# Kernel tuning notes

Measured on AMD Instinct MI355X. Metric: run time of the kernel, lower is better.

Reference implementation:

```python
import jax, jax.numpy as jnp
import numpy as np

DIM = 512
HEADS = 16
HD = DIM // HEADS            # head_dim = 32
WH, WW = 8, 8                # window_size
D0, D1 = 2, 2                # dilated_size
TWH, TWW = WH * D0, WW * D1  # total_window_size = 16,16
SCALE = HD ** -0.5


def _wpart(x, wh, ww):
    # (B,H,W,C) -> (B * H/wh * W/ww, wh, ww, C)
    B, H, W, C = x.shape
    x = x.reshape(B, H // wh, wh, W // ww, ww, C)
    return x.transpose(0, 1, 3, 2, 4, 5).reshape(-1, wh, ww, C)


def _wrev(win, wh, ww, H, W):
    # (nW*B, wh, ww, C) -> (B, H, W, C)
    C = win.shape[-1]
    B = win.shape[0] // ((H // wh) * (W // ww))
    x = win.reshape(B, H // wh, W // ww, wh, ww, C).transpose(0, 1, 3, 2, 4, 5)
    return x.reshape(B, H, W, C)


def _rope2(x):
    # 2D RoPE over a (B, WH, WW, HD) window: first half of HD rotated by row
    # position, second half by column position (axial rotary embedding).
    d = HD // 2
    inv = 1.0 / (10000.0 ** (jnp.arange(0, d, 2, dtype=jnp.float32) / d))  # (d/2,)

    def rot(xp, ang):
        x1, x2 = xp[..., 0::2], xp[..., 1::2]
        c, s = jnp.cos(ang), jnp.sin(ang)
        return jnp.stack([x1 * c - x2 * s, x1 * s + x2 * c], axis=-1).reshape(xp.shape)

    ah = (jnp.arange(WH, dtype=jnp.float32)[:, None] * inv)[:, None, :]  # (WH,1,d/2)
    aw = (jnp.arange(WW, dtype=jnp.float32)[:, None] * inv)[None, :, :]  # (1,WW,d/2)
    return jnp.concatenate([rot(x[..., :d], ah), rot(x[..., d:], aw)], axis=-1)


def _forward(x, qkv_w, qkv_b, proj_w, proj_b):
    B, H, W, C = x.shape
    # partition into total windows, then dilated regrouping
    xw = _wpart(x, TWH, TWW)                                   # (B_, 16, 16, C)
    B_ = xw.shape[0]
    xw = _wpart(xw, D0, D1)                                    # (B_*64, 2, 2, C)
    xw = xw.reshape(B_, WH * WW, D0 * D1, C)
    xw = xw.transpose(0, 2, 1, 3).reshape(B_ * D0 * D1, WH * WW, C)  # (B__, N, C)
    B__, N = xw.shape[0], xw.shape[1]

    qkv = (xw @ qkv_w.T + qkv_b).reshape(B__, N, 3, HEADS, HD).transpose(2, 0, 3, 1, 4)
    q, k, v = qkv[0], qkv[1], qkv[2]                           # (B__, HEADS, N, HD)

    q = _rope2(q.reshape(-1, WH, WW, HD)).reshape(B__, HEADS, N, HD) * SCALE
    k = _rope2(k.reshape(-1, WH, WW, HD)).reshape(B__, HEADS, N, HD)

    attn = jax.nn.softmax(jnp.einsum('bhnd,bhmd->bhnm', q, k), axis=-1)
    out = jnp.einsum('bhnm,bhmd->bhnd', attn, v)               # (B__, HEADS, N, HD)
    out = out.transpose(0, 2, 1, 3).reshape(B__, N, C)

    # undo dilated regrouping, then undo total-window partition
    out = out.reshape(B_, D0 * D1, N, C).transpose(0, 2, 1, 3).reshape(-1, D0, D1, C)
    out = _wrev(out, D0, D1, TWH, TWW)                         # (B_, 16, 16, C)
    out = _wrev(out, TWH, TWW, H, W)                           # (B, H, W, C)
    return out @ proj_w.T + proj_b


def setup_inputs() -> dict:
    key = jax.random.key(0)
    k0, k1, k2 = jax.random.split(key, 3)
    x = jax.random.normal(k0, (4, 128, 128, DIM), dtype=jnp.float32)
    qkv_w = jax.random.normal(k1, (3 * DIM, DIM), dtype=jnp.float32) * (DIM ** -0.5)
    qkv_b = jnp.zeros((3 * DIM,), dtype=jnp.float32)
    proj_w = jax.random.normal(k2, (DIM, DIM), dtype=jnp.float32) * (DIM ** -0.5)
    proj_b = jnp.zeros((DIM,), dtype=jnp.float32)
    return {"x": x, "qkv_w": qkv_w, "qkv_b": qkv_b, "proj_w": proj_w, "proj_b": proj_b}


def reference(x, qkv_w, qkv_b, proj_w, proj_b):
    return _forward(x, qkv_w, qkv_b, proj_w, proj_b)
```

## Files before the change

### kernel.cpp

```cpp
#include <hip/hip_runtime.h>
#include <hip/hip_bf16.h>
#include <stdint.h>

#define DIMC  512
#define NHEAD 16
#define HDIM  32
#define NTOK  65536
#define QKVN  1536
static constexpr float SCALE_F = 0.17677669529663687f;

typedef __attribute__((ext_vector_type(4))) float  f32x4;
typedef __attribute__((ext_vector_type(8))) __bf16 bf16x8;

__device__ __forceinline__ uint16_t f2bf(float f) {
  union { float f; uint32_t u; } v; v.f = f;
  return (uint16_t)((v.u + 0x7FFFu + ((v.u >> 16) & 1u)) >> 16);
}

__device__ __forceinline__ void gload_lds16(const void* g, void* l) {
  __builtin_amdgcn_global_load_lds((const __attribute__((address_space(1))) void*)g,
                                   (__attribute__((address_space(3))) void*)l,
                                   16, 0, 0);
}

__global__ void cvt_f32_bf16(const float* __restrict__ src,
                             uint16_t* __restrict__ dst, int n4)
{
  int i = blockIdx.x * blockDim.x + threadIdx.x;
  const int stride = gridDim.x * blockDim.x;
  for (; i < n4; i += stride) {
    const float4 v = ((const float4*)src)[i];
    ushort4 o;
    o.x = f2bf(v.x); o.y = f2bf(v.y); o.z = f2bf(v.z); o.w = f2bf(v.w);
    ((ushort4*)dst)[i] = o;
  }
}

template <bool OUT_F32>
__global__ __launch_bounds__(512, 2)
void gemm256_8ph(const uint16_t* __restrict__ A,
                 const uint16_t* __restrict__ B,
                 const float* __restrict__ bias,
                 void* __restrict__ Cv,
                 int M, int N, int K, int gx)
{
  __shared__ __align__(16) char lds[131072];

  const int tid = threadIdx.x;
  const int l  = tid & 63, w = tid >> 6;
  const int wm = w >> 2,  wn = w & 3;
  const int lm = l & 15,  lq = l >> 4;

  const int nwg = gridDim.x;
  const int qq = nwg >> 3, rr = nwg & 7;
  const int xcd = blockIdx.x & 7, loc = blockIdx.x >> 3;
  const int sw = (xcd < rr ? xcd * (qq + 1) : rr * (qq + 1) + (xcd - rr) * qq) + loc;
  const long m0 = (long)(sw / gx) * 256;
  const long n0 = (long)(sw % gx) * 256;

  const int srow  = tid >> 3;
  const int scolb = (((tid & 7) ^ (srow & 7)) << 4);
  const uint16_t* Ags = A + (m0 + srow) * (long)K + (scolb >> 1);
  const uint16_t* Bgs = B + (n0 + srow) * (long)K + (scolb >> 1);
  char* ldsW = lds + (w << 10);

  auto STAGE = [&](const uint16_t* Gs, int regionOff, int half, int kt) {
    const uint16_t* s0 = Gs + (size_t)(half * 128) * K + kt;
    gload_lds16(s0,                 ldsW + regionOff);
    gload_lds16(s0 + (size_t)64 * K, ldsW + regionOff + 8192);
  };

  const int colx0 = ((lq ^ (lm & 7)) << 4);
  const int aoff0 = (wm * 64 + lm) * 128 + colx0;
  const int aoff1 = (wm * 64 + lm) * 128 + (colx0 ^ 64);
  const int boff0 = (wn * 32 + lm) * 128 + colx0;
  const int boff1 = (wn * 32 + lm) * 128 + (colx0 ^ 64);

  f32x4 acc[2][2][4][2] = {};

#define PHASE(SLOT, QM, QN, STG, VM)                                          \
  {                                                                           \
    const char* Ab = lds + (SLOT) * 65536 + (QM) * 16384;                     \
    const char* Bb = lds + (SLOT) * 65536 + 32768 + (QN) * 16384;             \
    bf16x8 af0[4], af1[4], bq0[2], bq1[2];                                    \
    _Pragma("unroll") for (int i = 0; i < 4; ++i) {                           \
      af0[i] = *(const bf16x8*)(Ab + aoff0 + i * 2048);                       \
      af1[i] = *(const bf16x8*)(Ab + aoff1 + i * 2048);                       \
    }                                                                         \
    _Pragma("unroll") for (int j = 0; j < 2; ++j) {                           \
      bq0[j] = *(const bf16x8*)(Bb + boff0 + j * 2048);                       \
      bq1[j] = *(const bf16x8*)(Bb + boff1 + j * 2048);                       \
    }                                                                         \
    STG;                                                                      \
    __builtin_amdgcn_s_barrier();                                             \
    __builtin_amdgcn_s_setprio(1);                                            \
    _Pragma("unroll") for (int i = 0; i < 4; ++i)                             \
      _Pragma("unroll") for (int j = 0; j < 2; ++j) {                         \
        acc[QM][QN][i][j] = __builtin_amdgcn_mfma_f32_16x16x32_bf16(          \
            af0[i], bq0[j], acc[QM][QN][i][j], 0, 0, 0);                      \
        acc[QM][QN][i][j] = __builtin_amdgcn_mfma_f32_16x16x32_bf16(          \
            af1[i], bq1[j], acc[QM][QN][i][j], 0, 0, 0);                      \
      }                                                                       \
    __builtin_amdgcn_s_setprio(0);                                            \
    if (VM) { asm volatile("s_waitcnt vmcnt(4)" ::: "memory"); }              \
    __builtin_amdgcn_s_barrier();                                             \
  }

  STAGE(Ags, 0,             0, 0);
  STAGE(Bgs, 32768,         0, 0);
  STAGE(Ags, 16384,         1, 0);
  STAGE(Bgs, 49152,         1, 0);
  STAGE(Ags, 65536,         0, 64);
  STAGE(Bgs, 65536 + 32768, 0, 64);
  asm volatile("s_waitcnt vmcnt(4)" ::: "memory");
  __builtin_amdgcn_s_barrier();

  for (int t2 = 0; t2 < K / 64; t2 += 2) {
    const int k1 = (t2 + 1) * 64;
    int k2 = (t2 + 2) * 64; if (k2 >= K) k2 = 0;
    int k3 = (t2 + 3) * 64; if (k3 >= K) k3 = 0;
    PHASE(0, 0, 0, STAGE(Ags, 65536 + 16384, 1, k1), 0)
    PHASE(0, 0, 1, STAGE(Bgs, 65536 + 49152, 1, k1), 0)
    PHASE(0, 1, 0, STAGE(Ags, 0,             0, k2), 0)
    PHASE(0, 1, 1, STAGE(Bgs, 32768,         0, k2), 1)
    PHASE(1, 0, 0, STAGE(Ags, 16384,         1, k2), 0)
    PHASE(1, 0, 1, STAGE(Bgs, 49152,         1, k2), 0)
    PHASE(1, 1, 0, STAGE(Ags, 65536,         0, k3), 0)
    PHASE(1, 1, 1, STAGE(Bgs, 65536 + 32768, 0, k3), 1)
  }
#undef PHASE

#pragma unroll
  for (int qm = 0; qm < 2; ++qm)
#pragma unroll
  for (int qn = 0; qn < 2; ++qn)
#pragma unroll
  for (int i = 0; i < 4; ++i)
#pragma unroll
  for (int j = 0; j < 2; ++j) {
    const long m = m0 + qm * 128 + wm * 64 + i * 16 + lq * 4;
    const long n = n0 + qn * 128 + wn * 32 + j * 16 + lm;
    const float bv = bias[n];
#pragma unroll
    for (int r = 0; r < 4; ++r) {
      const float val = acc[qm][qn][i][j][r] + bv;
      if (OUT_F32) ((float*)Cv)[(m + r) * (long)N + n] = val;
      else         ((uint16_t*)Cv)[(m + r) * (long)N + n] = f2bf(val);
    }
  }
}

__global__ void attn_win(const uint16_t* __restrict__ QKV,
                         uint16_t* __restrict__ O)
{
  __shared__ __align__(16) __bf16 Pl[4][64][72];

  const int tid = threadIdx.x;
  const int l  = tid & 63, w = tid >> 6;
  const int lm = l & 15,  lq = l >> 4;
  const int bid = blockIdx.x;
  const int g = bid >> 2;
  const int h = (bid & 3) * 4 + w;

  const int d1 = g & 1, d0 = (g >> 1) & 1;
  const int wx = (g >> 2) & 7, wy = (g >> 5) & 7, bb = g >> 8;
  const long tbase = ((long)(bb * 128 + wy * 16 + d0) * 128) + wx * 16 + d1;

  f32x4 invs;
#pragma unroll
  for (int i = 0; i < 4; ++i)
    invs[i] = exp2f(-1.6609640474436813f * (float)((lq & 1) * 4 + i));

  const int co_q = h * HDIM;
  const int co_k = DIMC + h * HDIM;
  const int co_v = 2 * DIMC + h * HDIM;

  bf16x8 qf[4], kf[4];
#pragma unroll
  for (int f = 0; f < 4; ++f) {
    const int n  = f * 16 + lm;
    const int iy = n >> 3, ix = n & 7;
    const float pos = (lq < 2) ? (float)iy : (float)ix;
    const long t = tbase + iy * 256 + ix * 2;
    const uint16_t* qp = QKV + t * QKVN + co_q + lq * 8;
    const uint16_t* kp = QKV + t * QKVN + co_k + lq * 8;
    {
      bf16x8 raw = *(const bf16x8*)qp, o;
#pragma unroll
      for (int i = 0; i < 4; ++i) {
        float x1 = (float)raw[2 * i], x2 = (float)raw[2 * i + 1];
        float s, c; __sincosf(pos * invs[i], &s, &c);
        o[2 * i]     = (__bf16)((x1 * c - x2 * s) * SCALE_F);
        o[2 * i + 1] = (__bf16)((x1 * s + x2 * c) * SCALE_F);
      }
      qf[f] = o;
    }
    {
      bf16x8 raw = *(const bf16x8*)kp, o;
#pragma unroll
      for (int i = 0; i < 4; ++i) {
        float x1 = (float)raw[2 * i], x2 = (float)raw[2 * i + 1];
        float s, c; __sincosf(pos * invs[i], &s, &c);
        o[2 * i]     = (__bf16)(x1 * c - x2 * s);
        o[2 * i + 1] = (__bf16)(x1 * s + x2 * c);
      }
      kf[f] = o;
    }
  }

  const f32x4 fzero = {0.f, 0.f, 0.f, 0.f};
  f32x4 s[4][4];
#pragma unroll
  for (int mi = 0; mi < 4; ++mi)
#pragma unroll
    for (int ni = 0; ni < 4; ++ni)
      s[mi][ni] = __builtin_amdgcn_mfma_f32_16x16x32_bf16(qf[mi], kf[ni], fzero, 0, 0, 0);

  float rsum[4][4];
#pragma unroll
  for (int mi = 0; mi < 4; ++mi)
#pragma unroll
    for (int r = 0; r < 4; ++r) {
      float m = s[mi][0][r];
#pragma unroll
      for (int ni = 1; ni < 4; ++ni) m = fmaxf(m, s[mi][ni][r]);
      m = fmaxf(m, __shfl_xor(m, 1));
      m = fmaxf(m, __shfl_xor(m, 2));
      m = fmaxf(m, __shfl_xor(m, 4));
      m = fmaxf(m, __shfl_xor(m, 8));
      float sum = 0.f;
#pragma unroll
      for (int ni = 0; ni < 4; ++ni) {
        float p = expf(s[mi][ni][r] - m);
        s[mi][ni][r] = p;
        sum += p;
      }
      sum += __shfl_xor(sum, 1);
      sum += __shfl_xor(sum, 2);
      sum += __shfl_xor(sum, 4);
      sum += __shfl_xor(sum, 8);
      rsum[mi][r] = sum;
    }

#pragma unroll
  for (int mi = 0; mi < 4; ++mi)
#pragma unroll
    for (int ni = 0; ni < 4; ++ni)
#pragma unroll
      for (int r = 0; r < 4; ++r)
        Pl[w][mi * 16 + lq * 4 + r][ni * 16 + lm] = (__bf16)s[mi][ni][r];

  bf16x8 pa[4][2];
#pragma unroll
  for (int mi = 0; mi < 4; ++mi)
#pragma unroll
    for (int kk = 0; kk < 2; ++kk)
      pa[mi][kk] = *(const bf16x8*)(&Pl[w][mi * 16 + lm][kk * 32 + lq * 8]);

  bf16x8 vf[2][2];
#pragma unroll
  for (int kk = 0; kk < 2; ++kk)
#pragma unroll
    for (int n2 = 0; n2 < 2; ++n2) {
      const int nb = kk * 32 + lq * 8;
      const long tb2 = tbase + (long)(nb >> 3) * 256;
      const uint16_t* vp = QKV + co_v + n2 * 16 + lm;
      bf16x8 o;
#pragma unroll
      for (int i = 0; i < 8; ++i)
        o[i] = *(const __bf16*)(vp + (tb2 + 2 * i) * QKVN);
      vf[kk][n2] = o;
    }

  f32x4 oacc[4][2] = {};
#pragma unroll
  for (int kk = 0; kk < 2; ++kk)
#pragma unroll
    for (int mi = 0; mi < 4; ++mi)
#pragma unroll
      for (int n2 = 0; n2 < 2; ++n2)
        oacc[mi][n2] = __builtin_amdgcn_mfma_f32_16x16x32_bf16(
            pa[mi][kk], vf[kk][n2], oacc[mi][n2], 0, 0, 0);

#pragma unroll
  for (int mi = 0; mi < 4; ++mi)
#pragma unroll
    for (int r = 0; r < 4; ++r) {
      const int n = mi * 16 + lq * 4 + r;
      const long t = tbase + (n >> 3) * 256 + (n & 7) * 2;
      const float rinv = 1.0f / rsum[mi][r];
#pragma unroll
      for (int n2 = 0; n2 < 2; ++n2)
        O[t * DIMC + h * HDIM + n2 * 16 + lm] = f2bf(oacc[mi][n2][r] * rinv);
    }
}

extern "C" void kernel_launch(void* const* d_in, const int* in_sizes, int n_in,
                              void* d_out, int out_size, void* d_ws, size_t ws_size,
                              hipStream_t stream)
{
  const float* x      = (const float*)d_in[0];
  const float* qkv_w  = (const float*)d_in[1];
  const float* qkv_b  = (const float*)d_in[2];
  const float* proj_w = (const float*)d_in[3];
  const float* proj_b = (const float*)d_in[4];
  float* out = (float*)d_out;

  uint16_t* xb    = (uint16_t*)d_ws;
  uint16_t* qwb   = xb    + (size_t)NTOK * DIMC;
  uint16_t* pwb   = qwb   + (size_t)QKVN * DIMC;
  uint16_t* qkv   = pwb   + (size_t)DIMC * DIMC;
  uint16_t* attn  = qkv   + (size_t)NTOK * QKVN;

  cvt_f32_bf16<<<2048, 256, 0, stream>>>(x,      xb,  NTOK * DIMC / 4);
  cvt_f32_bf16<<<512,  256, 0, stream>>>(qkv_w,  qwb, QKVN * DIMC / 4);
  cvt_f32_bf16<<<256,  256, 0, stream>>>(proj_w, pwb, DIMC * DIMC / 4);

  gemm256_8ph<false><<<dim3((NTOK / 256) * (QKVN / 256)), dim3(512), 0, stream>>>(
      xb, qwb, qkv_b, qkv, NTOK, QKVN, DIMC, QKVN / 256);

  attn_win<<<dim3(1024 * 4), dim3(256), 0, stream>>>(qkv, attn);

  gemm256_8ph<true><<<dim3((NTOK / 256) * (DIMC / 256)), dim3(512), 0, stream>>>(
      attn, pwb, proj_b, out, NTOK, DIMC, DIMC, DIMC / 256);
}
```

Measured before the change: 304.2 us.

## Reuse LDS fragments across GEMM phases and prefetch them ahead of MFMA

Restructures the GEMM main loop so A and B fragments read from LDS are kept in registers and reused across the quadrant phases (2x2 subtiles), instead of every phase reloading both. Fragments for the next phase are read from LDS while the current MFMA block runs, which cuts LDS read traffic and overlaps it with compute. The vmcnt waits and barriers are re-placed to match the new order. In exchange, holding more fragment registers raises register pressure, and the hand-placed barrier/waitcnt schedule carries correctness risk.

```diff
diff --git a/kernel.cpp b/kernel.cpp
--- a/kernel.cpp
+++ b/kernel.cpp
@@ -64,11 +64,12 @@
   const uint16_t* Bgs = B + (n0 + srow) * (long)K + (scolb >> 1);
   char* ldsW = lds + (w << 10);
 
-  auto STAGE = [&](const uint16_t* Gs, int regionOff, int half, int kt) {
-    const uint16_t* s0 = Gs + (size_t)(half * 128) * K + kt;
-    gload_lds16(s0,                 ldsW + regionOff);
-    gload_lds16(s0 + (size_t)64 * K, ldsW + regionOff + 8192);
-  };
+#define STAGE(Gs, regionOff, half, kt)                                        \
+  {                                                                           \
+    const uint16_t* s0_ = (Gs) + (size_t)((half) * 128) * K + (kt);           \
+    gload_lds16(s0_,                  ldsW + (regionOff));                    \
+    gload_lds16(s0_ + (size_t)64 * K, ldsW + (regionOff) + 8192);             \
+  }
 
   const int colx0 = ((lq ^ (lm & 7)) << 4);
   const int aoff0 = (wm * 64 + lm) * 128 + colx0;
@@ -76,59 +77,71 @@
   const int boff0 = (wn * 32 + lm) * 128 + colx0;
   const int boff1 = (wn * 32 + lm) * 128 + (colx0 ^ 64);
 
-  f32x4 acc[2][2][4][2] = {};
-
-#define PHASE(SLOT, QM, QN, STG, VM)                                          \
-  {                                                                           \
-    const char* Ab = lds + (SLOT) * 65536 + (QM) * 16384;                     \
-    const char* Bb = lds + (SLOT) * 65536 + 32768 + (QN) * 16384;             \
-    bf16x8 af0[4], af1[4], bq0[2], bq1[2];                                    \
-    _Pragma("unroll") for (int i = 0; i < 4; ++i) {                           \
-      af0[i] = *(const bf16x8*)(Ab + aoff0 + i * 2048);                       \
-      af1[i] = *(const bf16x8*)(Ab + aoff1 + i * 2048);                       \
-    }                                                                         \
-    _Pragma("unroll") for (int j = 0; j < 2; ++j) {                           \
-      bq0[j] = *(const bf16x8*)(Bb + boff0 + j * 2048);                       \
-      bq1[j] = *(const bf16x8*)(Bb + boff1 + j * 2048);                       \
-    }                                                                         \
-    STG;                                                                      \
-    __builtin_amdgcn_s_barrier();                                             \
-    __builtin_amdgcn_s_setprio(1);                                            \
+  f32x4  acc[2][2][4][2] = {};
+  bf16x8 aX[4][2], aY[4][2];
+  bf16x8 b0[2][2], b1[2][2];
+
+#define RD_A(DST, OFF)                                                        \
+  _Pragma("unroll") for (int i = 0; i < 4; ++i) {                             \
+    DST[i][0] = *(const bf16x8*)(lds + (OFF) + aoff0 + i * 2048);             \
+    DST[i][1] = *(const bf16x8*)(lds + (OFF) + aoff1 + i * 2048);             \
+  }
+#define RD_B(DST, OFF)                                                        \
+  _Pragma("unroll") for (int j = 0; j < 2; ++j) {                             \
+    DST[j][0] = *(const bf16x8*)(lds + (OFF) + boff0 + j * 2048);             \
+    DST[j][1] = *(const bf16x8*)(lds + (OFF) + boff1 + j * 2048);             \
+  }
+#define MFMA16(AS, BS, QM, QN)                                                \
+  __builtin_amdgcn_s_setprio(1);                                              \
+  _Pragma("unroll") for (int kk = 0; kk < 2; ++kk)                            \
     _Pragma("unroll") for (int i = 0; i < 4; ++i)                             \
-      _Pragma("unroll") for (int j = 0; j < 2; ++j) {                         \
+      _Pragma("unroll") for (int j = 0; j < 2; ++j)                           \
         acc[QM][QN][i][j] = __builtin_amdgcn_mfma_f32_16x16x32_bf16(          \
-            af0[i], bq0[j], acc[QM][QN][i][j], 0, 0, 0);                      \
-        acc[QM][QN][i][j] = __builtin_amdgcn_mfma_f32_16x16x32_bf16(          \
-            af1[i], bq1[j], acc[QM][QN][i][j], 0, 0, 0);                      \
-      }                                                                       \
-    __builtin_amdgcn_s_setprio(0);                                            \
-    if (VM) { asm volatile("s_waitcnt vmcnt(4)" ::: "memory"); }              \
-    __builtin_amdgcn_s_barrier();                                             \
-  }
-
-  STAGE(Ags, 0,             0, 0);
-  STAGE(Bgs, 32768,         0, 0);
-  STAGE(Ags, 16384,         1, 0);
-  STAGE(Bgs, 49152,         1, 0);
-  STAGE(Ags, 65536,         0, 64);
-  STAGE(Bgs, 65536 + 32768, 0, 64);
-  asm volatile("s_waitcnt vmcnt(4)" ::: "memory");
-  __builtin_amdgcn_s_barrier();
+            AS[i][kk], BS[j][kk], acc[QM][QN][i][j], 0, 0, 0);                \
+  __builtin_amdgcn_s_setprio(0);
+#define VMW(N) asm volatile("s_waitcnt vmcnt(" #N ")" ::: "memory");
+#define BAR()  __builtin_amdgcn_s_barrier();
+
+  STAGE(Ags, 0,             0, 0)
+  STAGE(Bgs, 32768,         0, 0)
+  STAGE(Ags, 16384,         1, 0)
+  STAGE(Bgs, 49152,         1, 0)
+  STAGE(Ags, 65536,         0, 64)
+  STAGE(Bgs, 65536 + 32768, 0, 64)
+  VMW(8) BAR()
+  RD_A(aX, 0) RD_B(b0, 32768)
+  VMW(4) BAR()
 
   for (int t2 = 0; t2 < K / 64; t2 += 2) {
     const int k1 = (t2 + 1) * 64;
     int k2 = (t2 + 2) * 64; if (k2 >= K) k2 = 0;
     int k3 = (t2 + 3) * 64; if (k3 >= K) k3 = 0;
-    PHASE(0, 0, 0, STAGE(Ags, 65536 + 16384, 1, k1), 0)
-    PHASE(0, 0, 1, STAGE(Bgs, 65536 + 49152, 1, k1), 0)
-    PHASE(0, 1, 0, STAGE(Ags, 0,             0, k2), 0)
-    PHASE(0, 1, 1, STAGE(Bgs, 32768,         0, k2), 1)
-    PHASE(1, 0, 0, STAGE(Ags, 16384,         1, k2), 0)
-    PHASE(1, 0, 1, STAGE(Bgs, 49152,         1, k2), 0)
-    PHASE(1, 1, 0, STAGE(Ags, 65536,         0, k3), 0)
-    PHASE(1, 1, 1, STAGE(Bgs, 65536 + 32768, 0, k3), 1)
-  }
-#undef PHASE
+
+    RD_B(b1, 49152)                 STAGE(Ags, 65536 + 16384, 1, k1)
+    MFMA16(aX, b0, 0, 0)            BAR()
+    RD_A(aY, 16384)                 STAGE(Bgs, 65536 + 49152, 1, k1)
+    MFMA16(aX, b1, 0, 1)            BAR()
+    STAGE(Ags, 0, 0, k2)
+    MFMA16(aY, b0, 1, 0)            VMW(6) BAR()
+    RD_A(aX, 65536) RD_B(b0, 65536 + 32768)
+    STAGE(Bgs, 32768, 0, k2)
+    MFMA16(aY, b1, 1, 1)            VMW(4) BAR()
+    RD_B(b1, 65536 + 49152)         STAGE(Ags, 16384, 1, k2)
+    MFMA16(aX, b0, 0, 0)            BAR()
+    RD_A(aY, 65536 + 16384)         STAGE(Bgs, 49152, 1, k2)
+    MFMA16(aX, b1, 0, 1)            BAR()
+    STAGE(Ags, 65536, 0, k3)
+    MFMA16(aY, b0, 1, 0)            VMW(6) BAR()
+    RD_A(aX, 0) RD_B(b0, 32768)
+    STAGE(Bgs, 65536 + 32768, 0, k3)
+    MFMA16(aY, b1, 1, 1)            VMW(4) BAR()
+  }
+#undef STAGE
+#undef RD_A
+#undef RD_B
+#undef MFMA16
+#undef VMW
+#undef BAR
 
 #pragma unroll
   for (int qm = 0; qm < 2; ++qm)
```

After: 298.3 us. Within noise of the previous version (-1.9%).
